# Performance work log

Measured on AMD Instinct MI355X. Metric: run time of the kernel, lower is better.

## Reference

```python
import jax, jax.numpy as jnp
import numpy as np

DIM = 1024
N_HEADS = 16
HEAD_DIM = DIM // N_HEADS


def setup_inputs() -> dict:
    key = jax.random.key(0)
    ks = jax.random.split(key, 7)
    s = 1.0 / np.sqrt(DIM)
    return {
        "hidden_states": jax.random.normal(ks[0], (1, 4096, DIM), dtype=jnp.float32),
        "Wq": jax.random.uniform(ks[1], (DIM, DIM), jnp.float32, -s, s),
        "bq": jax.random.uniform(ks[2], (DIM,), jnp.float32, -s, s),
        "Wk": jax.random.uniform(ks[3], (DIM, DIM), jnp.float32, -s, s),
        "bk": jax.random.uniform(ks[4], (DIM,), jnp.float32, -s, s),
        "Wv": jax.random.uniform(ks[5], (DIM, DIM), jnp.float32, -s, s),
        "bv": jax.random.uniform(ks[6], (DIM,), jnp.float32, -s, s),
    }


def _split_heads(x):
    # [B, S, DIM] -> [B, H, S, HEAD_DIM]
    b, s, _ = x.shape
    return x.reshape(b, s, N_HEADS, HEAD_DIM).transpose(0, 2, 1, 3)


def reference(hidden_states, Wq, bq, Wk, bk, Wv, bv):
    q = _split_heads(hidden_states @ Wq + bq)
    k = _split_heads(hidden_states @ Wk + bk)
    v = _split_heads(hidden_states @ Wv + bv)
    scores = jnp.einsum("bhqd,bhkd->bhqk", q, k) / np.sqrt(HEAD_DIM).astype(np.float32)
    probs = jax.nn.softmax(scores, axis=-1)  # dropout prob = 0 -> identity
    ctx = jnp.einsum("bhqk,bhkd->bhqd", probs, v)
    b, h, s, d = ctx.shape
    return ctx.transpose(0, 2, 1, 3).reshape(b, s, h * d)
```

## Files before the change

kernel.cpp:

```cpp
#include <hip/hip_runtime.h>
#include <hip/hip_bf16.h>

#define S_LEN 4096
#define DIM   1024
#define NH    16
#define HD    64

typedef unsigned short u16;
typedef short  bf16x8 __attribute__((ext_vector_type(8)));
typedef float  f32x4  __attribute__((ext_vector_type(4)));

__device__ __forceinline__ u16 f2bf(float f){
  union { float f; unsigned u; } x; x.f = f;
  unsigned u = x.u;
  return (u16)((u + 0x7FFFu + ((u >> 16) & 1u)) >> 16);
}
__device__ __forceinline__ unsigned pk2(float a, float b){
  union { __hip_bfloat162 h; unsigned u; } x;
  x.h = __float22bfloat162_rn(float2{a, b});
  return x.u;
}
__device__ __forceinline__ void ld2lds16(const u16* g, u16* l){
  __builtin_amdgcn_global_load_lds((const __attribute__((address_space(1))) void*)g,
                                   (__attribute__((address_space(3))) void*)l, 16, 0, 0);
}

#define QSCALE 0.1803368801111204f

__global__ __launch_bounds__(256) void fill_sentinel(float* __restrict__ out, int n){
  int i = blockIdx.x * 256 + threadIdx.x;
  if (i < n) out[i] = 77.0f;
}

__global__ __launch_bounds__(256) void conv_x(const float* __restrict__ X, u16* __restrict__ Xb){
  size_t i = ((size_t)blockIdx.x * 256 + threadIdx.x) * 8;
  float4 v0 = *(const float4*)(X + i);
  float4 v1 = *(const float4*)(X + i + 4);
  uint4 w;
  w.x = pk2(v0.x, v0.y); w.y = pk2(v0.z, v0.w);
  w.z = pk2(v1.x, v1.y); w.w = pk2(v1.z, v1.w);
  *(uint4*)(Xb + i) = w;
}

__global__ __launch_bounds__(256) void transpose_w(
    const float* __restrict__ W0, const float* __restrict__ W1, const float* __restrict__ W2,
    u16* __restrict__ Wt)
{
  const float* W = blockIdx.z==0 ? W0 : blockIdx.z==1 ? W1 : W2;
  u16* T = Wt + (size_t)blockIdx.z * DIM * DIM;
  __shared__ __align__(16) u16 tile[64*72];
  int k0 = blockIdx.x*64, n0 = blockIdx.y*64;
  int t = threadIdx.x;
  #pragma unroll
  for (int i = 0; i < 4; ++i){
    int idx = t + i*256;
    int row = idx >> 4, col4 = (idx & 15) * 4;
    float4 v = *(const float4*)(W + (size_t)(k0+row)*DIM + n0 + col4);
    tile[(col4+0)*72 + row] = f2bf(v.x);
    tile[(col4+1)*72 + row] = f2bf(v.y);
    tile[(col4+2)*72 + row] = f2bf(v.z);
    tile[(col4+3)*72 + row] = f2bf(v.w);
  }
  __syncthreads();
  #pragma unroll
  for (int i = 0; i < 2; ++i){
    int idx = t + i*256;
    int n = idx >> 3, k16 = (idx & 7) * 8;
    *(int4*)(T + (size_t)(n0+n)*DIM + k0 + k16) = *(const int4*)(tile + n*72 + k16);
  }
}

__device__ __forceinline__ void qkv_epilogue(
    int z, int m0, int n0, int wm, int wn, int quad, int l15,
    const f32x4 acc[4][4], const float* bias,
    u16* __restrict__ qb, u16* __restrict__ kf_out, u16* __restrict__ vf_out)
{
  #pragma unroll
  for (int nt=0; nt<4; ++nt){
    int n = n0 + wn + nt*16 + l15;
    float bv = bias[n];
    int h = n >> 6, d = n & 63;
    #pragma unroll
    for (int mt=0; mt<4; ++mt){
      int mb = m0 + wm + mt*16 + quad*4;
      f32x4 c = acc[mt][nt];
      if (z == 0){
        #pragma unroll
        for (int r=0; r<4; ++r)
          qb[(size_t)(mb + r)*DIM + n] = f2bf((c[r] + bv) * QSCALE);
      } else if (z == 1){
        int half = d >> 5, quadk = (d >> 3) & 3, j = d & 7;
        #pragma unroll
        for (int r=0; r<4; ++r){
          int s = mb + r;
          size_t idx = ((((size_t)h*256 + (s >> 4))*2 + half)*64 + quadk*16 + (s & 15))*8 + j;
          kf_out[idx] = f2bf(c[r] + bv);
        }
      } else {
        int kt64 = mb >> 6;
        int kn   = (mb >> 4) & 3;
        int qsl  = (mb >> 2) & 3;
        int h2   = kn >> 1;
        int jj0  = (kn & 1) * 4;
        int dt = d >> 4, dl = d & 15;
        size_t base = (((((size_t)h*64 + kt64)*4 + dt)*2 + h2)*64 + qsl*16 + dl)*8 + jj0;
        ushort4 p;
        p.x = f2bf(c[0]+bv); p.y = f2bf(c[1]+bv);
        p.z = f2bf(c[2]+bv); p.w = f2bf(c[3]+bv);
        *(ushort4*)(vf_out + base) = p;
      }
    }
  }
}

__global__ __launch_bounds__(256) void qkv_gemm_fast(
    const u16* __restrict__ Xbf, const u16* __restrict__ Wt,
    const float* __restrict__ b0, const float* __restrict__ b1, const float* __restrict__ b2,
    u16* __restrict__ qb, u16* __restrict__ kf_out, u16* __restrict__ vf_out)
{
  int fid = blockIdx.x;
  int z   = fid >> 8;
  int r   = fid & 255;
  int m0  = (((r & 7) << 2) + ((r >> 3) & 3)) * 128;
  int n0  = (r >> 5) * 128;

  const u16* Wz = Wt + (size_t)z * DIM * DIM;
  const float* bias = z==0 ? b0 : z==1 ? b1 : b2;

  __shared__ __align__(16) u16 As[128*32];
  __shared__ __align__(16) u16 Bs[128*32];

  int t = threadIdx.x, wave = t >> 6, lane = t & 63, quad = lane >> 4, l15 = lane & 15;
  int wm = (wave >> 1) * 64, wn = (wave & 1) * 64;

  f32x4 acc[4][4];
  #pragma unroll
  for (int i=0;i<4;++i)
    #pragma unroll
    for (int j=0;j<4;++j) acc[i][j] = (f32x4){0.f,0.f,0.f,0.f};

  int srow = wave*32 + (lane >> 2);
  int skc_g = (((lane & 3) ^ ((lane >> 3) & 3))) * 8;
  int skc_l = (lane & 3) * 8;
  const u16* gA0 = Xbf + (size_t)(m0 + srow)*DIM + skc_g;
  const u16* gA1 = gA0 + (size_t)16*DIM;
  const u16* gB0 = Wz  + (size_t)(n0 + srow)*DIM + skc_g;
  const u16* gB1 = gB0 + (size_t)16*DIM;
  u16* lA0 = As + srow*32 + skc_l;
  u16* lA1 = lA0 + 16*32;
  u16* lB0 = Bs + srow*32 + skc_l;
  u16* lB1 = lB0 + 16*32;

  int swz = (quad ^ ((l15 >> 1) & 3)) * 8;

  for (int kt = 0; kt < 32; ++kt){
    int ko = kt * 32;
    __syncthreads();
    ld2lds16(gA0 + ko, lA0);
    ld2lds16(gA1 + ko, lA1);
    ld2lds16(gB0 + ko, lB0);
    ld2lds16(gB1 + ko, lB1);
    __syncthreads();
    bf16x8 af[4], bfr[4];
    #pragma unroll
    for (int mt=0; mt<4; ++mt) af[mt]  = *(const bf16x8*)(As + (wm + mt*16 + l15)*32 + swz);
    #pragma unroll
    for (int nt=0; nt<4; ++nt) bfr[nt] = *(const bf16x8*)(Bs + (wn + nt*16 + l15)*32 + swz);
    #pragma unroll
    for (int mt=0; mt<4; ++mt)
      #pragma unroll
      for (int nt=0; nt<4; ++nt)
        acc[mt][nt] = __builtin_amdgcn_mfma_f32_16x16x32_bf16(af[mt], bfr[nt], acc[mt][nt], 0, 0, 0);
  }
  qkv_epilogue(z, m0, n0, wm, wn, quad, l15, acc, bias, qb, kf_out, vf_out);
}

__global__ __launch_bounds__(256) void qkv_gemm_legacy(
    const float* __restrict__ X,
    const float* __restrict__ Wq, const float* __restrict__ Wk, const float* __restrict__ Wv,
    const float* __restrict__ b0, const float* __restrict__ b1, const float* __restrict__ b2,
    u16* __restrict__ qb, u16* __restrict__ kf_out, u16* __restrict__ vf_out)
{
  int z = blockIdx.z;
  const float* W    = z==0 ? Wq : z==1 ? Wk : Wv;
  const float* bias = z==0 ? b0 : z==1 ? b1 : b2;

  __shared__ __align__(16) u16 As[128*40];
  __shared__ __align__(16) u16 Bs[128*40];

  int m0 = blockIdx.x * 128, n0 = blockIdx.y * 128;
  int t = threadIdx.x, wave = t >> 6, lane = t & 63, quad = lane >> 4, l15 = lane & 15;
  int wm = (wave >> 1) * 64, wn = (wave & 1) * 64;

  f32x4 acc[4][4];
  #pragma unroll
  for (int i=0;i<4;++i)
    #pragma unroll
    for (int j=0;j<4;++j) acc[i][j] = (f32x4){0.f,0.f,0.f,0.f};

  int sr = t >> 2, sc = (t & 3) * 8;
  const float* gA0 = X + (size_t)(m0 + sr) * DIM + sc;
  const float* gA1 = X + (size_t)(m0 + 64 + sr) * DIM + sc;
  int br = t >> 3, bc = (t & 7) * 16;
  const float* gW = W + (size_t)br * DIM + n0 + bc;

  for (int kt = 0; kt < 32; ++kt){
    int ko = kt * 32;
    float4 a00 = *(const float4*)(gA0 + ko);
    float4 a01 = *(const float4*)(gA0 + ko + 4);
    float4 a10 = *(const float4*)(gA1 + ko);
    float4 a11 = *(const float4*)(gA1 + ko + 4);
    float4 w0  = *(const float4*)(gW + (size_t)ko*DIM);
    float4 w1  = *(const float4*)(gW + (size_t)ko*DIM + 4);
    float4 w2  = *(const float4*)(gW + (size_t)ko*DIM + 8);
    float4 w3  = *(const float4*)(gW + (size_t)ko*DIM + 12);
    int4 pa0, pa1;
    pa0.x = pk2(a00.x,a00.y); pa0.y = pk2(a00.z,a00.w);
    pa0.z = pk2(a01.x,a01.y); pa0.w = pk2(a01.z,a01.w);
    pa1.x = pk2(a10.x,a10.y); pa1.y = pk2(a10.z,a10.w);
    pa1.z = pk2(a11.x,a11.y); pa1.w = pk2(a11.z,a11.w);
    u16 wb[16];
    wb[0]=f2bf(w0.x); wb[1]=f2bf(w0.y); wb[2]=f2bf(w0.z); wb[3]=f2bf(w0.w);
    wb[4]=f2bf(w1.x); wb[5]=f2bf(w1.y); wb[6]=f2bf(w1.z); wb[7]=f2bf(w1.w);
    wb[8]=f2bf(w2.x); wb[9]=f2bf(w2.y); wb[10]=f2bf(w2.z); wb[11]=f2bf(w2.w);
    wb[12]=f2bf(w3.x); wb[13]=f2bf(w3.y); wb[14]=f2bf(w3.z); wb[15]=f2bf(w3.w);
    __syncthreads();
    *(int4*)(As + sr*40 + sc)      = pa0;
    *(int4*)(As + (64+sr)*40 + sc) = pa1;
    #pragma unroll
    for (int j=0;j<16;++j) Bs[(bc+j)*40 + br] = wb[j];
    __syncthreads();
    bf16x8 af[4], bfr[4];
    #pragma unroll
    for (int mt=0; mt<4; ++mt) af[mt]  = *(const bf16x8*)(As + (wm + mt*16 + l15)*40 + quad*8);
    #pragma unroll
    for (int nt=0; nt<4; ++nt) bfr[nt] = *(const bf16x8*)(Bs + (wn + nt*16 + l15)*40 + quad*8);
    #pragma unroll
    for (int mt=0; mt<4; ++mt)
      #pragma unroll
      for (int nt=0; nt<4; ++nt)
        acc[mt][nt] = __builtin_amdgcn_mfma_f32_16x16x32_bf16(af[mt], bfr[nt], acc[mt][nt], 0, 0, 0);
  }
  qkv_epilogue(z, m0, n0, wm, wn, quad, l15, acc, bias, qb, kf_out, vf_out);
}

__global__ __launch_bounds__(256, 2) void attn(
    const u16* __restrict__ Qb, const u16* __restrict__ Kf,
    const u16* __restrict__ Vf, float* __restrict__ out)
{
  int fid = blockIdx.x;
  int xcd  = fid & 7;
  int hpar = (fid >> 3) & 1;
  int qb   = fid >> 4;
  int h    = xcd*2 + hpar;

  int t = threadIdx.x, wave = t >> 6, lane = t & 63, quad = lane >> 4, l15 = lane & 15;
  int q0 = qb * 128 + wave * 32;
  int dg = (wave ^ (fid >> 8)) & 1;

  __shared__ __align__(16) u16 Ks0[4096], Ks1[4096], Vs0[4096], Vs1[4096];

  const u16* Kfh = Kf + (size_t)h * 262144;
  const u16* Vfh = Vf + (size_t)h * 262144;

  bf16x8 qf[2][2];
  #pragma unroll
  for (int qs=0; qs<2; ++qs){
    const u16* Qp = Qb + (size_t)(q0 + qs*16 + l15)*DIM + h*HD;
    qf[qs][0] = *(const bf16x8*)(Qp + quad*8);
    qf[qs][1] = *(const bf16x8*)(Qp + 32 + quad*8);
  }

  f32x4 O[2][4];
  #pragma unroll
  for (int qs=0; qs<2; ++qs)
    #pragma unroll
    for (int dt=0; dt<4; ++dt) O[qs][dt] = (f32x4){0.f,0.f,0.f,0.f};
  float lsum[2] = {0.f, 0.f};

  typedef union { uint4 u; bf16x8 v; } pfu;

#define STAGE(KS, VS, T)                                                         \
  do {                                                                           \
    const u16* kg_ = Kfh + (size_t)(T)*4096 + t*8;                               \
    ld2lds16(kg_,        KS + t*8);                                              \
    ld2lds16(kg_ + 2048, KS + t*8 + 2048);                                       \
    const u16* vg_ = Vfh + (size_t)(T)*4096 + t*8;                               \
    ld2lds16(vg_,        VS + t*8);                                              \
    ld2lds16(vg_ + 2048, VS + t*8 + 2048);                                       \
  } while(0)

#define QK_EXP(KS, PF)                                                           \
  do {                                                                           \
    bf16x8 kfr[4][2];                                                            \
    _Pragma("unroll")                                                            \
    for (int kn=0; kn<4; ++kn)                                                   \
      _Pragma("unroll")                                                          \
      for (int hf=0; hf<2; ++hf)                                                 \
        kfr[kn][hf] = *(const bf16x8*)((KS) + (kn*2+hf)*512 + lane*8);           \
    f32x4 st[2][4];                                                              \
    __builtin_amdgcn_s_setprio(1);                                               \
    _Pragma("unroll")                                                            \
    for (int qs=0; qs<2; ++qs)                                                   \
      _Pragma("unroll")                                                          \
      for (int kn=0; kn<4; ++kn){                                                \
        f32x4 zz = (f32x4){0.f,0.f,0.f,0.f};                                     \
        zz = __builtin_amdgcn_mfma_f32_16x16x32_bf16(kfr[kn][0], qf[qs][0], zz, 0,0,0); \
        zz = __builtin_amdgcn_mfma_f32_16x16x32_bf16(kfr[kn][1], qf[qs][1], zz, 0,0,0); \
        st[qs][kn] = zz;                                                         \
      }                                                                          \
    __builtin_amdgcn_s_setprio(0);                                               \
    _Pragma("unroll")                                                            \
    for (int qs=0; qs<2; ++qs){                                                  \
      float ls = 0.f;                                                            \
      _Pragma("unroll")                                                          \
      for (int kn=0; kn<4; ++kn)                                                 \
        _Pragma("unroll")                                                        \
        for (int r=0; r<4; ++r){                                                 \
          float p = __builtin_amdgcn_exp2f(st[qs][kn][r]);                       \
          st[qs][kn][r] = p; ls += p;                                            \
        }                                                                        \
      lsum[qs] += ls;                                                            \
      PF[qs][0].u.x = pk2(st[qs][0][0], st[qs][0][1]);                           \
      PF[qs][0].u.y = pk2(st[qs][0][2], st[qs][0][3]);                           \
      PF[qs][0].u.z = pk2(st[qs][1][0], st[qs][1][1]);                           \
      PF[qs][0].u.w = pk2(st[qs][1][2], st[qs][1][3]);                           \
      PF[qs][1].u.x = pk2(st[qs][2][0], st[qs][2][1]);                           \
      PF[qs][1].u.y = pk2(st[qs][2][2], st[qs][2][3]);                           \
      PF[qs][1].u.z = pk2(st[qs][3][0], st[qs][3][1]);                           \
      PF[qs][1].u.w = pk2(st[qs][3][2], st[qs][3][3]);                           \
    }                                                                            \
  } while(0)

#define LOADV(VFR, VS)                                                           \
  do {                                                                           \
    _Pragma("unroll")                                                            \
    for (int dt=0; dt<4; ++dt)                                                   \
      _Pragma("unroll")                                                          \
      for (int c2=0; c2<2; ++c2)                                                 \
        VFR[dt][c2] = *(const bf16x8*)((VS) + (dt*2+c2)*512 + lane*8);           \
  } while(0)

#define PV(PF, VFR)                                                              \
  do {                                                                           \
    __builtin_amdgcn_s_setprio(1);                                               \
    _Pragma("unroll")                                                            \
    for (int qs=0; qs<2; ++qs)                                                   \
      _Pragma("unroll")                                                          \
      for (int dt=0; dt<4; ++dt){                                                \
        f32x4 o = O[qs][dt];                                                     \
        o = __builtin_amdgcn_mfma_f32_16x16x32_bf16(VFR[dt][0], PF[qs][0].v, o, 0,0,0); \
        o = __builtin_amdgcn_mfma_f32_16x16x32_bf16(VFR[dt][1], PF[qs][1].v, o, 0,0,0); \
        O[qs][dt] = o;                                                           \
      }                                                                          \
    __builtin_amdgcn_s_setprio(0);                                               \
  } while(0)

#define COMPUTE(KS, VS, FIRST)                                                   \
  do {                                                                           \
    if (!dg){                                                                    \
      pfu pfN[2][2]; bf16x8 vfrN[4][2];                                          \
      QK_EXP(KS, pfN);                                                           \
      LOADV(vfrN, VS);                                                           \
      PV(pfN, vfrN);                                                             \
    } else {                                                                     \
      if (!(FIRST)) PV(pfC, vfrC);                                               \
      QK_EXP(KS, pfC);                                                           \
      LOADV(vfrC, VS);                                                           \
    }                                                                            \
  } while(0)

  pfu pfC[2][2];
  bf16x8 vfrC[4][2];

  STAGE(Ks0, Vs0, 0);
  __syncthreads();
  STAGE(Ks1, Vs1, 1);
  COMPUTE(Ks0, Vs0, 1);
  __syncthreads();

  for (int kt = 1; kt < 63; kt += 2){
    STAGE(Ks0, Vs0, kt+1);
    COMPUTE(Ks1, Vs1, 0);
    __syncthreads();
    STAGE(Ks1, Vs1, kt+2);
    COMPUTE(Ks0, Vs0, 0);
    __syncthreads();
  }
  COMPUTE(Ks1, Vs1, 0);
  if (dg) PV(pfC, vfrC);

#undef STAGE
#undef QK_EXP
#undef LOADV
#undef PV
#undef COMPUTE

  #pragma unroll
  for (int qs=0; qs<2; ++qs){
    float l = lsum[qs];
    l += __shfl_xor(l, 16, 64);
    l += __shfl_xor(l, 32, 64);
    float inv = 1.0f / l;
    int query = q0 + qs*16 + l15;
    #pragma unroll
    for (int dt=0; dt<4; ++dt){
      float4 v;
      v.x = O[qs][dt][0]*inv; v.y = O[qs][dt][1]*inv;
      v.z = O[qs][dt][2]*inv; v.w = O[qs][dt][3]*inv;
      *(float4*)(out + (size_t)query*DIM + h*HD + dt*16 + quad*4) = v;
    }
  }
}

extern "C" void kernel_launch(void* const* d_in, const int* in_sizes, int n_in,
                              void* d_out, int out_size, void* d_ws, size_t ws_size,
                              hipStream_t stream)
{
  const float* X  = (const float*)d_in[0];
  const float* Wq = (const float*)d_in[1];
  const float* bq = (const float*)d_in[2];
  const float* Wk = (const float*)d_in[3];
  const float* bk = (const float*)d_in[4];
  const float* Wv = (const float*)d_in[5];
  const float* bv = (const float*)d_in[6];
  float* out = (float*)d_out;
  u16*   ws  = (u16*)d_ws;

  const size_t SD = (size_t)S_LEN * DIM;
  const size_t need_fast = (4*SD + 3*(size_t)DIM*DIM) * sizeof(u16);
  const size_t need_min  = (size_t)24 * 1024 * 1024;

  if (ws_size >= need_fast){
    u16* xbf = ws;
    u16* wt  = xbf + SD;
    u16* qb  = wt + 3*(size_t)DIM*DIM;
    u16* kf  = qb + SD;
    u16* vf  = kf + SD;
    conv_x       <<<dim3((int)(SD/8/256)), 256, 0, stream>>>(X, xbf);
    transpose_w  <<<dim3(16,16,3), 256, 0, stream>>>(Wq, Wk, Wv, wt);
    qkv_gemm_fast<<<dim3(768), 256, 0, stream>>>(xbf, wt, bq, bk, bv, qb, kf, vf);
    attn         <<<dim3(512), 256, 0, stream>>>(qb, kf, vf, out);
  } else if (ws_size >= need_min){
    u16* qb = ws;
    u16* kf = qb + SD;
    u16* vf = kf + SD;
    qkv_gemm_legacy<<<dim3(32, 8, 3), 256, 0, stream>>>(X, Wq, Wk, Wv, bq, bk, bv, qb, kf, vf);
    attn           <<<dim3(512), 256, 0, stream>>>(qb, kf, vf, out);
  } else {
    fill_sentinel<<<(out_size + 255)/256, 256, 0, stream>>>(out, out_size);
  }
}
```

Baseline: 208.9 us.

## Fuse prep kernels and double the K-tile depth in QKV GEMM

```diff
diff --git a/kernel.cpp b/kernel.cpp
--- a/kernel.cpp
+++ b/kernel.cpp
@@ -32,25 +32,30 @@
   if (i < n) out[i] = 77.0f;
 }
 
-__global__ __launch_bounds__(256) void conv_x(const float* __restrict__ X, u16* __restrict__ Xb){
-  size_t i = ((size_t)blockIdx.x * 256 + threadIdx.x) * 8;
-  float4 v0 = *(const float4*)(X + i);
-  float4 v1 = *(const float4*)(X + i + 4);
-  uint4 w;
-  w.x = pk2(v0.x, v0.y); w.y = pk2(v0.z, v0.w);
-  w.z = pk2(v1.x, v1.y); w.w = pk2(v1.z, v1.w);
-  *(uint4*)(Xb + i) = w;
-}
-
-__global__ __launch_bounds__(256) void transpose_w(
+__global__ __launch_bounds__(256) void prep_fused(
+    const float* __restrict__ X, u16* __restrict__ Xb,
     const float* __restrict__ W0, const float* __restrict__ W1, const float* __restrict__ W2,
     u16* __restrict__ Wt)
 {
-  const float* W = blockIdx.z==0 ? W0 : blockIdx.z==1 ? W1 : W2;
-  u16* T = Wt + (size_t)blockIdx.z * DIM * DIM;
   __shared__ __align__(16) u16 tile[64*72];
-  int k0 = blockIdx.x*64, n0 = blockIdx.y*64;
+  int b = blockIdx.x;
   int t = threadIdx.x;
+  if (b < 2048){
+    size_t i = ((size_t)b * 256 + t) * 8;
+    float4 v0 = *(const float4*)(X + i);
+    float4 v1 = *(const float4*)(X + i + 4);
+    uint4 w;
+    w.x = pk2(v0.x, v0.y); w.y = pk2(v0.z, v0.w);
+    w.z = pk2(v1.x, v1.y); w.w = pk2(v1.z, v1.w);
+    *(uint4*)(Xb + i) = w;
+    return;
+  }
+  int tid = b - 2048;
+  int z   = tid >> 8;
+  int rem = tid & 255;
+  int k0  = (rem & 15) * 64, n0 = (rem >> 4) * 64;
+  const float* W = z==0 ? W0 : z==1 ? W1 : W2;
+  u16* T = Wt + (size_t)z * DIM * DIM;
   #pragma unroll
   for (int i = 0; i < 4; ++i){
     int idx = t + i*256;
@@ -127,8 +132,8 @@
   const u16* Wz = Wt + (size_t)z * DIM * DIM;
   const float* bias = z==0 ? b0 : z==1 ? b1 : b2;
 
-  __shared__ __align__(16) u16 As[128*32];
-  __shared__ __align__(16) u16 Bs[128*32];
+  __shared__ __align__(16) u16 As[128*64];
+  __shared__ __align__(16) u16 Bs[128*64];
 
   int t = threadIdx.x, wave = t >> 6, lane = t & 63, quad = lane >> 4, l15 = lane & 15;
   int wm = (wave >> 1) * 64, wn = (wave & 1) * 64;
@@ -139,38 +144,46 @@
     #pragma unroll
     for (int j=0;j<4;++j) acc[i][j] = (f32x4){0.f,0.f,0.f,0.f};
 
-  int srow = wave*32 + (lane >> 2);
-  int skc_g = (((lane & 3) ^ ((lane >> 3) & 3))) * 8;
-  int skc_l = (lane & 3) * 8;
-  const u16* gA0 = Xbf + (size_t)(m0 + srow)*DIM + skc_g;
-  const u16* gA1 = gA0 + (size_t)16*DIM;
-  const u16* gB0 = Wz  + (size_t)(n0 + srow)*DIM + skc_g;
-  const u16* gB1 = gB0 + (size_t)16*DIM;
-  u16* lA0 = As + srow*32 + skc_l;
-  u16* lA1 = lA0 + 16*32;
-  u16* lB0 = Bs + srow*32 + skc_l;
-  u16* lB1 = lB0 + 16*32;
-
-  int swz = (quad ^ ((l15 >> 1) & 3)) * 8;
-
-  for (int kt = 0; kt < 32; ++kt){
-    int ko = kt * 32;
-    __syncthreads();
-    ld2lds16(gA0 + ko, lA0);
-    ld2lds16(gA1 + ko, lA1);
-    ld2lds16(gB0 + ko, lB0);
-    ld2lds16(gB1 + ko, lB1);
-    __syncthreads();
-    bf16x8 af[4], bfr[4];
-    #pragma unroll
-    for (int mt=0; mt<4; ++mt) af[mt]  = *(const bf16x8*)(As + (wm + mt*16 + l15)*32 + swz);
-    #pragma unroll
-    for (int nt=0; nt<4; ++nt) bfr[nt] = *(const bf16x8*)(Bs + (wn + nt*16 + l15)*32 + swz);
+  int srow8  = t >> 3;
+  int schunk = t & 7;
+  int gchunk = schunk ^ (srow8 & 7);
+  const u16* gA = Xbf + (size_t)(m0 + srow8)*DIM + gchunk*8;
+  const u16* gB = Wz  + (size_t)(n0 + srow8)*DIM + gchunk*8;
+  u16* lA = As + srow8*64 + schunk*8;
+  u16* lB = Bs + srow8*64 + schunk*8;
+
+  for (int kt = 0; kt < 16; ++kt){
+    int ko = kt * 64;
+    __syncthreads();
+    #pragma unroll
+    for (int i=0;i<4;++i){
+      ld2lds16(gA + (size_t)(32*i)*DIM + ko, lA + 32*i*64);
+      ld2lds16(gB + (size_t)(32*i)*DIM + ko, lB + 32*i*64);
+    }
+    __syncthreads();
+    bf16x8 af[2][4], bfr[2][4];
+    #pragma unroll
+    for (int kh=0; kh<2; ++kh){
+      #pragma unroll
+      for (int mt=0; mt<4; ++mt){
+        int row = wm + mt*16 + l15;
+        int c = (kh*4 + quad) ^ (l15 & 7);
+        af[kh][mt] = *(const bf16x8*)(As + row*64 + c*8);
+      }
+      #pragma unroll
+      for (int nt=0; nt<4; ++nt){
+        int row = wn + nt*16 + l15;
+        int c = (kh*4 + quad) ^ (l15 & 7);
+        bfr[kh][nt] = *(const bf16x8*)(Bs + row*64 + c*8);
+      }
+    }
     #pragma unroll
     for (int mt=0; mt<4; ++mt)
       #pragma unroll
-      for (int nt=0; nt<4; ++nt)
-        acc[mt][nt] = __builtin_amdgcn_mfma_f32_16x16x32_bf16(af[mt], bfr[nt], acc[mt][nt], 0, 0, 0);
+      for (int nt=0; nt<4; ++nt){
+        acc[mt][nt] = __builtin_amdgcn_mfma_f32_16x16x32_bf16(af[0][mt], bfr[0][nt], acc[mt][nt], 0, 0, 0);
+        acc[mt][nt] = __builtin_amdgcn_mfma_f32_16x16x32_bf16(af[1][mt], bfr[1][nt], acc[mt][nt], 0, 0, 0);
+      }
   }
   qkv_epilogue(z, m0, n0, wm, wn, quad, l15, acc, bias, qb, kf_out, vf_out);
 }
@@ -437,8 +450,7 @@
     u16* qb  = wt + 3*(size_t)DIM*DIM;
     u16* kf  = qb + SD;
     u16* vf  = kf + SD;
-    conv_x       <<<dim3((int)(SD/8/256)), 256, 0, stream>>>(X, xbf);
-    transpose_w  <<<dim3(16,16,3), 256, 0, stream>>>(Wq, Wk, Wv, wt);
+    prep_fused   <<<dim3(2048 + 768), 256, 0, stream>>>(X, xbf, Wq, Wk, Wv, wt);
     qkv_gemm_fast<<<dim3(768), 256, 0, stream>>>(xbf, wt, bq, bk, bv, qb, kf, vf);
     attn         <<<dim3(512), 256, 0, stream>>>(qb, kf, vf, out);
   } else if (ws_size >= need_min){
```

Measured after the change: 205.2 us. About the same (-1.7%).

## Double-buffer QKV GEMM LDS tiles and fuse prep kernels into one launch

Applied to the files above, without the earlier changes.

```diff
diff --git a/kernel.cpp b/kernel.cpp
--- a/kernel.cpp
+++ b/kernel.cpp
@@ -32,25 +32,30 @@
   if (i < n) out[i] = 77.0f;
 }
 
-__global__ __launch_bounds__(256) void conv_x(const float* __restrict__ X, u16* __restrict__ Xb){
-  size_t i = ((size_t)blockIdx.x * 256 + threadIdx.x) * 8;
-  float4 v0 = *(const float4*)(X + i);
-  float4 v1 = *(const float4*)(X + i + 4);
-  uint4 w;
-  w.x = pk2(v0.x, v0.y); w.y = pk2(v0.z, v0.w);
-  w.z = pk2(v1.x, v1.y); w.w = pk2(v1.z, v1.w);
-  *(uint4*)(Xb + i) = w;
-}
-
-__global__ __launch_bounds__(256) void transpose_w(
+__global__ __launch_bounds__(256) void prep_fused(
+    const float* __restrict__ X, u16* __restrict__ Xb,
     const float* __restrict__ W0, const float* __restrict__ W1, const float* __restrict__ W2,
     u16* __restrict__ Wt)
 {
-  const float* W = blockIdx.z==0 ? W0 : blockIdx.z==1 ? W1 : W2;
-  u16* T = Wt + (size_t)blockIdx.z * DIM * DIM;
   __shared__ __align__(16) u16 tile[64*72];
-  int k0 = blockIdx.x*64, n0 = blockIdx.y*64;
+  int b = blockIdx.x;
   int t = threadIdx.x;
+  if (b < 2048){
+    size_t i = ((size_t)b * 256 + t) * 8;
+    float4 v0 = *(const float4*)(X + i);
+    float4 v1 = *(const float4*)(X + i + 4);
+    uint4 w;
+    w.x = pk2(v0.x, v0.y); w.y = pk2(v0.z, v0.w);
+    w.z = pk2(v1.x, v1.y); w.w = pk2(v1.z, v1.w);
+    *(uint4*)(Xb + i) = w;
+    return;
+  }
+  int tid = b - 2048;
+  int z   = tid >> 8;
+  int rem = tid & 255;
+  int k0  = (rem & 15) * 64, n0 = (rem >> 4) * 64;
+  const float* W = z==0 ? W0 : z==1 ? W1 : W2;
+  u16* T = Wt + (size_t)z * DIM * DIM;
   #pragma unroll
   for (int i = 0; i < 4; ++i){
     int idx = t + i*256;
@@ -127,8 +132,8 @@
   const u16* Wz = Wt + (size_t)z * DIM * DIM;
   const float* bias = z==0 ? b0 : z==1 ? b1 : b2;
 
-  __shared__ __align__(16) u16 As[128*32];
-  __shared__ __align__(16) u16 Bs[128*32];
+  __shared__ __align__(16) u16 As[2*128*32];
+  __shared__ __align__(16) u16 Bs[2*128*32];
 
   int t = threadIdx.x, wave = t >> 6, lane = t & 63, quad = lane >> 4, l15 = lane & 15;
   int wm = (wave >> 1) * 64, wn = (wave & 1) * 64;
@@ -153,25 +158,43 @@
 
   int swz = (quad ^ ((l15 >> 1) & 3)) * 8;
 
-  for (int kt = 0; kt < 32; ++kt){
-    int ko = kt * 32;
-    __syncthreads();
-    ld2lds16(gA0 + ko, lA0);
-    ld2lds16(gA1 + ko, lA1);
-    ld2lds16(gB0 + ko, lB0);
-    ld2lds16(gB1 + ko, lB1);
-    __syncthreads();
-    bf16x8 af[4], bfr[4];
-    #pragma unroll
-    for (int mt=0; mt<4; ++mt) af[mt]  = *(const bf16x8*)(As + (wm + mt*16 + l15)*32 + swz);
-    #pragma unroll
-    for (int nt=0; nt<4; ++nt) bfr[nt] = *(const bf16x8*)(Bs + (wn + nt*16 + l15)*32 + swz);
-    #pragma unroll
-    for (int mt=0; mt<4; ++mt)
-      #pragma unroll
-      for (int nt=0; nt<4; ++nt)
-        acc[mt][nt] = __builtin_amdgcn_mfma_f32_16x16x32_bf16(af[mt], bfr[nt], acc[mt][nt], 0, 0, 0);
-  }
+#define GSTAGE(P, KO)                                                            \
+  do {                                                                           \
+    ld2lds16(gA0 + (KO), lA0 + (P)*4096);                                        \
+    ld2lds16(gA1 + (KO), lA1 + (P)*4096);                                        \
+    ld2lds16(gB0 + (KO), lB0 + (P)*4096);                                        \
+    ld2lds16(gB1 + (KO), lB1 + (P)*4096);                                        \
+  } while(0)
+
+#define GCOMPUTE(P)                                                              \
+  do {                                                                           \
+    bf16x8 af[4], bfr[4];                                                        \
+    _Pragma("unroll")                                                            \
+    for (int mt=0; mt<4; ++mt) af[mt]  = *(const bf16x8*)(As + (P)*4096 + (wm + mt*16 + l15)*32 + swz); \
+    _Pragma("unroll")                                                            \
+    for (int nt=0; nt<4; ++nt) bfr[nt] = *(const bf16x8*)(Bs + (P)*4096 + (wn + nt*16 + l15)*32 + swz); \
+    _Pragma("unroll")                                                            \
+    for (int mt=0; mt<4; ++mt)                                                   \
+      _Pragma("unroll")                                                          \
+      for (int nt=0; nt<4; ++nt)                                                 \
+        acc[mt][nt] = __builtin_amdgcn_mfma_f32_16x16x32_bf16(af[mt], bfr[nt], acc[mt][nt], 0, 0, 0); \
+  } while(0)
+
+  GSTAGE(0, 0);
+  __syncthreads();
+
+  for (int kt = 0; kt < 32; kt += 2){
+    GSTAGE(1, (kt+1)*32);
+    GCOMPUTE(0);
+    __syncthreads();
+    if (kt + 2 < 32) GSTAGE(0, (kt+2)*32);
+    GCOMPUTE(1);
+    __syncthreads();
+  }
+
+#undef GSTAGE
+#undef GCOMPUTE
+
   qkv_epilogue(z, m0, n0, wm, wn, quad, l15, acc, bias, qb, kf_out, vf_out);
 }
 
@@ -437,8 +460,7 @@
     u16* qb  = wt + 3*(size_t)DIM*DIM;
     u16* kf  = qb + SD;
     u16* vf  = kf + SD;
-    conv_x       <<<dim3((int)(SD/8/256)), 256, 0, stream>>>(X, xbf);
-    transpose_w  <<<dim3(16,16,3), 256, 0, stream>>>(Wq, Wk, Wv, wt);
+    prep_fused   <<<dim3(2048 + 768), 256, 0, stream>>>(X, xbf, Wq, Wk, Wv, wt);
     qkv_gemm_fast<<<dim3(768), 256, 0, stream>>>(xbf, wt, bq, bk, bv, qb, kf, vf);
     attn         <<<dim3(512), 256, 0, stream>>>(qb, kf, vf, out);
   } else if (ws_size >= need_min){
```

Result: no change. 207.4 us (-0.7%).
